# Kernel optimization log

Measured on AMD Instinct MI355X. Metric: run time of the kernel, lower is better.

Reference implementation:

```python
import jax, jax.numpy as jnp
import numpy as np

UNITS = 1024
D_Q = 1024
D_V = 1024


def setup_inputs() -> dict:
    key = jax.random.key(0)
    ks = jax.random.split(key, 8)
    B, S = 32, 2048
    query = jax.random.normal(ks[0], (B, D_Q), dtype=jnp.float32)
    values = jax.random.normal(ks[1], (B, S, D_V), dtype=jnp.float32)
    # Keras Dense params (glorot-ish scale for weights, zero bias init kept random-free)
    W1 = jax.random.normal(ks[2], (D_V, UNITS), dtype=jnp.float32) / np.sqrt(D_V)
    b1 = jnp.zeros((UNITS,), dtype=jnp.float32)
    W2 = jax.random.normal(ks[3], (D_Q, UNITS), dtype=jnp.float32) / np.sqrt(D_Q)
    b2 = jnp.zeros((UNITS,), dtype=jnp.float32)
    V = jax.random.normal(ks[4], (UNITS, 1), dtype=jnp.float32) / np.sqrt(UNITS)
    bV = jnp.zeros((1,), dtype=jnp.float32)
    return {"query": query, "values": values, "W1": W1, "b1": b1,
            "W2": W2, "b2": b2, "V": V, "bV": bV}


def reference(query, values, W1, b1, W2, b2, V, bV):
    # query: [B, d_q], values: [B, S, d_v]
    proj_v = jnp.einsum('bsd,du->bsu', values, W1) + b1        # [B, S, U]
    proj_q = (query @ W2 + b2)[:, None, :]                      # [B, 1, U]
    score = jnp.tanh(proj_v + proj_q) @ V + bV                  # [B, S, 1]
    attention_weights = jax.nn.softmax(score, axis=1)           # [B, S, 1]
    context_vector = jnp.sum(attention_weights * values, axis=1)  # [B, d_v]
    return (context_vector, attention_weights)
```

## Files before the change

### kernel.cpp

```cpp
#include <hip/hip_runtime.h>
#include <math.h>

#define B_  32
#define S_  2048
#define DV  1024
#define U_  1024

typedef __attribute__((ext_vector_type(8))) short bf16x8;
typedef __attribute__((ext_vector_type(4))) float f32x4;

__device__ inline unsigned short f2bf(float f) {
    unsigned int x = __float_as_uint(f);
    return (unsigned short)((x + 0x7fffu + ((x >> 16) & 1u)) >> 16);
}

__device__ inline float tanh_fast(float x) {
    float ax = fabsf(x);
    float e  = __expf(ax + ax);
    float t  = 1.0f - __fdividef(2.0f, e + 1.0f);
    return copysignf(t, x);
}

__device__ __forceinline__ void gload16(const void* g, void* l) {
    __builtin_amdgcn_global_load_lds(
        (const __attribute__((address_space(1))) void*)g,
        (__attribute__((address_space(3))) void*)l,
        16, 0, 0);
}

#define ASM_VMCNT(N) asm volatile("s_waitcnt vmcnt(" #N ")" ::: "memory")
#define ASM_LGKM0()  do { asm volatile("s_waitcnt lgkmcnt(0)" ::: "memory"); \
                          __builtin_amdgcn_sched_barrier(0); } while (0)

__global__ __launch_bounds__(256)
void fused_prep(const float* __restrict__ values, char* __restrict__ AbfT,
                const float* __restrict__ W1, unsigned short* __restrict__ W1T,
                const float* __restrict__ query, const float* __restrict__ W2,
                const float* __restrict__ b1, const float* __restrict__ b2,
                float* __restrict__ t, float* __restrict__ scores,
                float* __restrict__ ctx) {
    const int bid = blockIdx.x;
    const int tid = threadIdx.x;

    if (bid < 32768) {
        size_t i = ((size_t)bid * 256 + tid) * 8;
        int row = (int)(i >> 10);
        int k   = (int)(i & 1023);
        float4 f0 = *(const float4*)(values + i);
        float4 f1 = *(const float4*)(values + i + 4);
        union { unsigned short s[8]; uint4 u; } p;
        p.s[0] = f2bf(f0.x); p.s[1] = f2bf(f0.y); p.s[2] = f2bf(f0.z); p.s[3] = f2bf(f0.w);
        p.s[4] = f2bf(f1.x); p.s[5] = f2bf(f1.y); p.s[6] = f2bf(f1.z); p.s[7] = f2bf(f1.w);
        int stile = row >> 8, rt = row & 255, h = rt >> 7, r = rt & 127;
        int kt = k >> 6, kk = k & 63;
        int pchunk = (kk >> 3) ^ (r & 7);
        size_t dst = (size_t)stile * 524288 + (size_t)kt * 32768
                   + h * 16384 + r * 128 + pchunk * 16;
        *(uint4*)(AbfT + dst) = p.u;
    } else if (bid < 33024) {
        __shared__ float tile[64][65];
        int i = bid - 32768;
        int k0 = (i & 15) * 64, u0 = (i >> 4) * 64;
        int lr = tid >> 4, lc = (tid & 15) * 4;
#pragma unroll
        for (int j = 0; j < 4; ++j) {
            float4 f = *(const float4*)&W1[(size_t)(k0 + lr + j * 16) * U_ + u0 + lc];
            tile[lr + j * 16][lc + 0] = f.x; tile[lr + j * 16][lc + 1] = f.y;
            tile[lr + j * 16][lc + 2] = f.z; tile[lr + j * 16][lc + 3] = f.w;
        }
        __syncthreads();
        int ur = tid >> 2, kq = (tid & 3) * 16;
        union { unsigned short s[8]; uint4 u; } p0, p1;
#pragma unroll
        for (int e = 0; e < 8; ++e) p0.s[e] = f2bf(tile[kq + e][ur]);
#pragma unroll
        for (int e = 0; e < 8; ++e) p1.s[e] = f2bf(tile[kq + 8 + e][ur]);
        unsigned short* dst = W1T + (size_t)(u0 + ur) * 1024 + k0 + kq;
        *(uint4*)dst       = p0.u;
        *(uint4*)(dst + 8) = p1.u;
    } else if (bid < 33152) {
        __shared__ float qs2[1024];
        int i = bid - 33024;
        int b = i >> 2, uq = i & 3;
        for (int j = tid; j < 1024; j += 256) qs2[j] = query[b * DV + j];
        __syncthreads();
        int u = uq * 256 + tid;
        float a0 = 0.f, a1 = 0.f, a2 = 0.f, a3 = 0.f;
        float a4 = 0.f, a5 = 0.f, a6 = 0.f, a7 = 0.f;
        const float* w = W2 + u;
        for (int k = 0; k < 1024; k += 8) {
            a0 += qs2[k + 0] * w[(size_t)(k + 0) * U_];
            a1 += qs2[k + 1] * w[(size_t)(k + 1) * U_];
            a2 += qs2[k + 2] * w[(size_t)(k + 2) * U_];
            a3 += qs2[k + 3] * w[(size_t)(k + 3) * U_];
            a4 += qs2[k + 4] * w[(size_t)(k + 4) * U_];
            a5 += qs2[k + 5] * w[(size_t)(k + 5) * U_];
            a6 += qs2[k + 6] * w[(size_t)(k + 6) * U_];
            a7 += qs2[k + 7] * w[(size_t)(k + 7) * U_];
        }
        t[b * U_ + u] = b1[u] + b2[u]
                      + ((a0 + a1) + (a2 + a3)) + ((a4 + a5) + (a6 + a7));
    } else if (bid < 33408) {
        scores[(bid - 33152) * 256 + tid] = 0.f;
    } else {
        ctx[(bid - 33408) * 256 + tid] = 0.f;
    }
}

#define MFMA16(MB, NB)                                                          \
    _Pragma("unroll") for (int ks = 0; ks < 2; ++ks)                            \
    _Pragma("unroll") for (int n = 0; n < 2; ++n)                               \
    _Pragma("unroll") for (int m = 0; m < 4; ++m)                               \
        acc[(MB)+m][(NB)+n] = __builtin_amdgcn_mfma_f32_16x16x32_bf16(          \
            af[m][ks], bf[n][ks], acc[(MB)+m][(NB)+n], 0, 0, 0);

__launch_bounds__(512, 2)
__global__ void scores_mfma8(const char* __restrict__ AbfT,
                             const unsigned short* __restrict__ W1T,
                             const float* __restrict__ tvec,
                             const float* __restrict__ V,
                             float* __restrict__ scores) {
    __shared__ __align__(16) char lds[131072];

    const int tid  = threadIdx.x;
    const int lane = tid & 63;
    const int wave = tid >> 6;
    const int wm   = wave >> 2;
    const int wn   = wave & 3;
    const int l15  = lane & 15;
    const int lq   = lane >> 4;

    const int id    = blockIdx.x;
    const int wg    = (id & 7) * 128 + (id >> 3);
    const int utile = wg & 3;
    const int stile = wg >> 2;
    const size_t row0 = (size_t)stile * 256;
    const int b       = (int)(row0 >> 11);
    const int s_local = (int)(row0 & 2047);
    const int u0      = utile * 256;

    const char* aBase = AbfT + (size_t)stile * 524288 + wave * 1024 + lane * 16;
    const int rowst = wave * 8 + (lane >> 3);
    const int kch8  = ((lane & 7) ^ ((lane >> 3) & 7)) * 8;
    const unsigned short* bSrc = W1T + (size_t)(u0 + rowst) * 1024 + kch8;
    char* const dstW = lds + wave * 1024;

    const int ao0 = wm * 16384 + l15 * 128 + ((lq ^ (l15 & 7)) << 4);
    const int ao1 = ao0 ^ 64;
    const int bo0 = 32768 + (wn >> 1) * 16384 + (wn & 1) * 8192
                  + l15 * 128 + ((lq ^ (l15 & 7)) << 4);
    const int bo1 = bo0 ^ 64;

    f32x4 acc[8][4];
#pragma unroll
    for (int m = 0; m < 8; ++m)
#pragma unroll
        for (int n = 0; n < 4; ++n) acc[m][n] = (f32x4)0.f;

    bf16x8 af[4][2];
    bf16x8 bf[2][2];

    auto stageA = [&](size_t gOff, int dOff) {
        gload16(aBase + gOff,        dstW + dOff);
        gload16(aBase + gOff + 8192, dstW + dOff + 8192);
    };
    auto stageB = [&](const unsigned short* s, int dOff) {
        gload16(s,             dstW + dOff);
        gload16(s + 64 * 1024, dstW + dOff + 8192);
    };
    auto readA4 = [&](int base) {
#pragma unroll
        for (int m = 0; m < 4; ++m) {
            af[m][0] = *(const bf16x8*)(lds + base + m * 2048 + ao0);
            af[m][1] = *(const bf16x8*)(lds + base + m * 2048 + ao1);
        }
    };
    auto readB2 = [&](int base) {
#pragma unroll
        for (int n = 0; n < 2; ++n) {
            bf[n][0] = *(const bf16x8*)(lds + base + n * 2048 + bo0);
            bf[n][1] = *(const bf16x8*)(lds + base + n * 2048 + bo1);
        }
    };

    stageA(0,     0);
    stageA(16384, 16384);
    stageB(bSrc,          32768);
    stageB(bSrc + 131072, 49152);
    stageA(32768, 65536);
    __builtin_amdgcn_sched_barrier(0);
    ASM_VMCNT(2);
    __builtin_amdgcn_s_barrier();
    __builtin_amdgcn_sched_barrier(0);

    for (int it = 0; it < 8; ++it) {
        const bool pf = (it < 7);
        const size_t aIt = (size_t)it * 65536;
        readA4(0);
        readB2(0);
        stageA(aIt + 49152, 81920);
        __builtin_amdgcn_s_barrier();
        ASM_LGKM0();
        __builtin_amdgcn_s_setprio(1);
        MFMA16(0, 0);
        __builtin_amdgcn_s_setprio(0);
        __builtin_amdgcn_s_barrier();
        readB2(2 * 2048);
        stageB(bSrc + 64, 98304);
        __builtin_amdgcn_s_barrier();
        ASM_LGKM0();
        __builtin_amdgcn_s_setprio(1);
        MFMA16(0, 2);
        __builtin_amdgcn_s_setprio(0);
        __builtin_amdgcn_s_barrier();
        readA4(4 * 2048);
        stageB(bSrc + 64 + 131072, 114688);
        __builtin_amdgcn_s_barrier();
        ASM_LGKM0();
        __builtin_amdgcn_s_setprio(1);
        MFMA16(4, 2);
        __builtin_amdgcn_s_setprio(0);
        __builtin_amdgcn_s_barrier();
        readB2(0);
        if (pf) stageA(aIt + 65536, 0);
        __builtin_amdgcn_s_barrier();
        ASM_LGKM0();
        __builtin_amdgcn_s_setprio(1);
        MFMA16(4, 0);
        __builtin_amdgcn_s_setprio(0);
        __builtin_amdgcn_sched_barrier(0);
        if (pf) { ASM_VMCNT(2); } else { ASM_VMCNT(0); }
        __builtin_amdgcn_s_barrier();
        __builtin_amdgcn_sched_barrier(0);
        readA4(65536);
        readB2(65536);
        if (pf) stageA(aIt + 81920, 16384);
        __builtin_amdgcn_s_barrier();
        ASM_LGKM0();
        __builtin_amdgcn_s_setprio(1);
        MFMA16(0, 0);
        __builtin_amdgcn_s_setprio(0);
        __builtin_amdgcn_s_barrier();
        readB2(65536 + 2 * 2048);
        if (pf) stageB(bSrc + 128, 32768);
        __builtin_amdgcn_s_barrier();
        ASM_LGKM0();
        __builtin_amdgcn_s_setprio(1);
        MFMA16(0, 2);
        __builtin_amdgcn_s_setprio(0);
        __builtin_amdgcn_s_barrier();
        readA4(65536 + 4 * 2048);
        if (pf) stageB(bSrc + 128 + 131072, 49152);
        __builtin_amdgcn_s_barrier();
        ASM_LGKM0();
        __builtin_amdgcn_s_setprio(1);
        MFMA16(4, 2);
        __builtin_amdgcn_s_setprio(0);
        __builtin_amdgcn_s_barrier();
        readB2(65536);
        if (pf) stageA(aIt + 98304, 65536);
        __builtin_amdgcn_s_barrier();
        ASM_LGKM0();
        __builtin_amdgcn_s_setprio(1);
        MFMA16(4, 0);
        __builtin_amdgcn_s_setprio(0);
        __builtin_amdgcn_sched_barrier(0);
        if (pf) { ASM_VMCNT(2); }
        __builtin_amdgcn_s_barrier();
        __builtin_amdgcn_sched_barrier(0);

        bSrc += 128;
    }

    __syncthreads();
    float* fscore = (float*)lds;
    if (tid < 256) fscore[tid] = 0.f;
    __syncthreads();
    float tu[4], vu[4];
#pragma unroll
    for (int n = 0; n < 4; ++n) {
        int u = u0 + wn * 64 + n * 16 + l15;
        tu[n] = tvec[b * U_ + u];
        vu[n] = V[u];
    }
#pragma unroll
    for (int m = 0; m < 8; ++m) {
#pragma unroll
        for (int r = 0; r < 4; ++r) {
            float p = 0.f;
#pragma unroll
            for (int n = 0; n < 4; ++n) p += tanh_fast(acc[m][n][r] + tu[n]) * vu[n];
            p += __shfl_xor(p, 1);
            p += __shfl_xor(p, 2);
            p += __shfl_xor(p, 4);
            p += __shfl_xor(p, 8);
            if (l15 == 0) atomicAdd(&fscore[wm * 128 + m * 16 + lq * 4 + r], p);
        }
    }
    __syncthreads();
    if (tid < 256) atomicAdd(&scores[(size_t)b * S_ + s_local + tid], fscore[tid]);
}

__global__ __launch_bounds__(256)
void fused_sm_ctx(const float* __restrict__ scores, const float* __restrict__ values,
                  float* __restrict__ wout, float* __restrict__ ctx) {
    const int b   = blockIdx.x;
    const int sc  = blockIdx.y;
    const int tid = threadIdx.x;
    __shared__ float red[256];
    __shared__ float ws_[128];

    float v[8];
    float m = -1e30f;
#pragma unroll
    for (int i = 0; i < 8; ++i) {
        v[i] = scores[(size_t)b * S_ + tid + i * 256];
        m = fmaxf(m, v[i]);
    }
    red[tid] = m; __syncthreads();
    for (int off = 128; off > 0; off >>= 1) {
        if (tid < off) red[tid] = fmaxf(red[tid], red[tid + off]);
        __syncthreads();
    }
    m = red[0];
    __syncthreads();
    float s = 0.f;
#pragma unroll
    for (int i = 0; i < 8; ++i) s += __expf(v[i] - m);
    red[tid] = s; __syncthreads();
    for (int off = 128; off > 0; off >>= 1) {
        if (tid < off) red[tid] += red[tid + off];
        __syncthreads();
    }
    float inv = 1.f / red[0];
    __syncthreads();

    if (tid < 128) {
        float x = scores[(size_t)b * S_ + sc * 128 + tid];
        float w = __expf(x - m) * inv;
        ws_[tid] = w;
        wout[(size_t)b * S_ + sc * 128 + tid] = w;
    }
    __syncthreads();

    const float4* vp = (const float4*)(values + ((size_t)b * S_ + sc * 128) * DV) + tid;
    float ax = 0.f, ay = 0.f, az = 0.f, aw = 0.f;
#pragma unroll 4
    for (int s2 = 0; s2 < 128; ++s2) {
        float4 vv = vp[(size_t)s2 * 256];
        float wv = ws_[s2];
        ax += wv * vv.x; ay += wv * vv.y; az += wv * vv.z; aw += wv * vv.w;
    }
    float* c = ctx + b * DV + tid * 4;
    atomicAdd(c + 0, ax); atomicAdd(c + 1, ay);
    atomicAdd(c + 2, az); atomicAdd(c + 3, aw);
}

__global__ void init_kernel(const float* __restrict__ b1, const float* __restrict__ b2,
                            float* __restrict__ t, float* __restrict__ ctx,
                            float* __restrict__ scores) {
    int i = blockIdx.x * 256 + threadIdx.x;
    scores[i] = 0.f;
    if (i < B_ * U_) {
        int u = i & (U_ - 1);
        t[i]   = b1[u] + b2[u];
        ctx[i] = 0.f;
    }
}

__global__ void projq_kernel(const float* __restrict__ q, const float* __restrict__ W2,
                             float* __restrict__ t) {
    int b  = blockIdx.x;
    int ks = blockIdx.y;
    int tid = threadIdx.x;
    __shared__ float qs[64];
    if (tid < 64) qs[tid] = q[b * DV + ks * 64 + tid];
    __syncthreads();
    float a0 = 0.f, a1 = 0.f, a2 = 0.f, a3 = 0.f;
    const float* w = W2 + (size_t)(ks * 64) * U_;
    for (int d = 0; d < 64; ++d) {
        float qd = qs[d];
        const float* wr = w + (size_t)d * U_ + tid;
        a0 += qd * wr[0];
        a1 += qd * wr[256];
        a2 += qd * wr[512];
        a3 += qd * wr[768];
    }
    atomicAdd(&t[b * U_ + tid      ], a0);
    atomicAdd(&t[b * U_ + tid + 256], a1);
    atomicAdd(&t[b * U_ + tid + 512], a2);
    atomicAdd(&t[b * U_ + tid + 768], a3);
}

__global__ void prep_w1t(const float* __restrict__ W1, unsigned short* __restrict__ W1T) {
    __shared__ float tile[64][65];
    int k0 = blockIdx.x * 64, u0 = blockIdx.y * 64;
    int t = threadIdx.x;
    int lr = t >> 4, lc = (t & 15) * 4;
#pragma unroll
    for (int i = 0; i < 4; ++i) {
        float4 f = *(const float4*)&W1[(size_t)(k0 + lr + i * 16) * U_ + u0 + lc];
        tile[lr + i * 16][lc + 0] = f.x; tile[lr + i * 16][lc + 1] = f.y;
        tile[lr + i * 16][lc + 2] = f.z; tile[lr + i * 16][lc + 3] = f.w;
    }
    __syncthreads();
    int ur = t >> 2, kq = (t & 3) * 16;
    union { unsigned short s[8]; uint4 u; } p0, p1;
#pragma unroll
    for (int e = 0; e < 8; ++e) p0.s[e] = f2bf(tile[kq + e][ur]);
#pragma unroll
    for (int e = 0; e < 8; ++e) p1.s[e] = f2bf(tile[kq + 8 + e][ur]);
    unsigned short* dst = W1T + (size_t)(u0 + ur) * 1024 + k0 + kq;
    *(uint4*)dst       = p0.u;
    *(uint4*)(dst + 8) = p1.u;
}

template<bool ABF16>
__launch_bounds__(256, 2)
__global__ void scores_mfma(const void* __restrict__ aPtr,
                            const unsigned short* __restrict__ W1T,
                            const float* __restrict__ t,
                            const float* __restrict__ V,
                            float* __restrict__ scores) {
    __shared__ unsigned short sA[128 * 40];
    __shared__ unsigned short sB[256 * 40];
    __shared__ float fscore[128];

    const int tid  = threadIdx.x;
    const int lane = tid & 63;
    const int wave = tid >> 6;
    const int wm = wave & 1, wn = wave >> 1;
    const int l15 = lane & 15, lq = lane >> 4;

    const int id    = blockIdx.x;
    const int utile = (id >> 3) & 3;
    const int stile = (id & 7) | ((id >> 5) << 3);
    const size_t row0 = (size_t)stile * 128;
    const int b       = (int)(row0 >> 11);
    const int s_local = (int)(row0 & 2047);
    const int u0      = utile * 256;

    if (tid < 128) fscore[tid] = 0.f;

    const int ar = tid >> 1, ak = (tid & 1) << 4;
    const int br = tid >> 1, bk = (tid & 1) << 4;

    const float* Af = (const float*)aPtr + (row0 + ar) * 1024 + ak;
    const unsigned short* Ab = (const unsigned short*)aPtr + (row0 + ar) * 1024 + ak;
    const unsigned short* Bp0 = W1T + (size_t)(u0 + br) * 1024 + bk;
    const unsigned short* Bp1 = Bp0 + 128 * 1024;

    f32x4 acc[4][8];
#pragma unroll
    for (int i = 0; i < 4; ++i)
#pragma unroll
        for (int j = 0; j < 8; ++j) acc[i][j] = (f32x4)0.f;

    uint4 sa0, sa1, sb0, sb1, sb2, sb3;
    float4 fa0, fa1, fa2, fa3;

    if (ABF16) {
        sa0 = *(const uint4*)(Ab);
        sa1 = *(const uint4*)(Ab + 8);
    } else {
        fa0 = *(const float4*)(Af);
        fa1 = *(const float4*)(Af + 4);
        fa2 = *(const float4*)(Af + 8);
        fa3 = *(const float4*)(Af + 12);
    }
    sb0 = *(const uint4*)(Bp0);
    sb1 = *(const uint4*)(Bp0 + 8);
    sb2 = *(const uint4*)(Bp1);
    sb3 = *(const uint4*)(Bp1 + 8);

    for (int k0 = 0; k0 < 1024; k0 += 32) {
        __syncthreads();
        if (ABF16) {
            *(uint4*)&sA[ar * 40 + ak]     = sa0;
            *(uint4*)&sA[ar * 40 + ak + 8] = sa1;
        } else {
            union { unsigned short s[8]; uint4 u; } p0, p1;
            p0.s[0] = f2bf(fa0.x); p0.s[1] = f2bf(fa0.y); p0.s[2] = f2bf(fa0.z); p0.s[3] = f2bf(fa0.w);
            p0.s[4] = f2bf(fa1.x); p0.s[5] = f2bf(fa1.y); p0.s[6] = f2bf(fa1.z); p0.s[7] = f2bf(fa1.w);
            p1.s[0] = f2bf(fa2.x); p1.s[1] = f2bf(fa2.y); p1.s[2] = f2bf(fa2.z); p1.s[3] = f2bf(fa2.w);
            p1.s[4] = f2bf(fa3.x); p1.s[5] = f2bf(fa3.y); p1.s[6] = f2bf(fa3.z); p1.s[7] = f2bf(fa3.w);
            *(uint4*)&sA[ar * 40 + ak]     = p0.u;
            *(uint4*)&sA[ar * 40 + ak + 8] = p1.u;
        }
        *(uint4*)&sB[br * 40 + bk]           = sb0;
        *(uint4*)&sB[br * 40 + bk + 8]       = sb1;
        *(uint4*)&sB[(br + 128) * 40 + bk]     = sb2;
        *(uint4*)&sB[(br + 128) * 40 + bk + 8] = sb3;

        if (k0 + 32 < 1024) {
            int nk = k0 + 32;
            if (ABF16) {
                sa0 = *(const uint4*)(Ab + nk);
                sa1 = *(const uint4*)(Ab + nk + 8);
            } else {
                fa0 = *(const float4*)(Af + nk);
                fa1 = *(const float4*)(Af + nk + 4);
                fa2 = *(const float4*)(Af + nk + 8);
                fa3 = *(const float4*)(Af + nk + 12);
            }
            sb0 = *(const uint4*)(Bp0 + nk);
            sb1 = *(const uint4*)(Bp0 + nk + 8);
            sb2 = *(const uint4*)(Bp1 + nk);
            sb3 = *(const uint4*)(Bp1 + nk + 8);
        }
        __syncthreads();

        bf16x8 af[4];
#pragma unroll
        for (int i = 0; i < 4; ++i)
            af[i] = *(const bf16x8*)&sA[(64 * wm + 16 * i + l15) * 40 + lq * 8];
#pragma unroll
        for (int j = 0; j < 8; ++j) {
            bf16x8 bfj = *(const bf16x8*)&sB[(128 * wn + 16 * j + l15) * 40 + lq * 8];
#pragma unroll
            for (int i = 0; i < 4; ++i)
                acc[i][j] = __builtin_amdgcn_mfma_f32_16x16x32_bf16(af[i], bfj, acc[i][j], 0, 0, 0);
        }
    }

    float tu[8], vu[8];
#pragma unroll
    for (int j = 0; j < 8; ++j) {
        int u = u0 + 128 * wn + 16 * j + l15;
        tu[j] = t[b * U_ + u];
        vu[j] = V[u];
    }
#pragma unroll
    for (int i = 0; i < 4; ++i) {
#pragma unroll
        for (int r = 0; r < 4; ++r) {
            float p = 0.f;
#pragma unroll
            for (int j = 0; j < 8; ++j) p += tanh_fast(acc[i][j][r] + tu[j]) * vu[j];
            p += __shfl_xor(p, 1);
            p += __shfl_xor(p, 2);
            p += __shfl_xor(p, 4);
            p += __shfl_xor(p, 8);
            if (l15 == 0) atomicAdd(&fscore[64 * wm + 16 * i + lq * 4 + r], p);
        }
    }
    __syncthreads();
    if (tid < 128) atomicAdd(&scores[(size_t)b * S_ + s_local + tid], fscore[tid]);
}

__launch_bounds__(256, 2)
__global__ void scores_vec(const float* __restrict__ values, const float* __restrict__ W1,
                           const float* __restrict__ t, const float* __restrict__ V,
                           float* __restrict__ scores) {
    __shared__ float vA[16][132];
    __shared__ float vB[16][68];
    __shared__ float fscore[128];
    const int b   = blockIdx.y;
    const int s0  = blockIdx.x * 128;
    const int tid = threadIdx.x;
    const int tx  = tid & 15, ty = tid >> 4;
    if (tid < 128) fscore[tid] = 0.f;
    const float* vbase = values + ((size_t)b * S_ + s0) * (size_t)DV;
    const int lm = tid >> 2, lkq = (tid & 3) * 4;
    const int lbk = tid >> 4, lbj = (tid & 15) * 4;
    for (int nt = 0; nt < U_ / 64; ++nt) {
        const int u0 = nt * 64;
        float acc[8][4];
#pragma unroll
        for (int i = 0; i < 8; ++i)
#pragma unroll
            for (int j = 0; j < 4; ++j) acc[i][j] = 0.f;
        for (int k0 = 0; k0 < DV; k0 += 16) {
            __syncthreads();
            const float4 v0 = *(const float4*)(vbase + (size_t)lm * DV + k0 + lkq);
            const float4 v1 = *(const float4*)(vbase + (size_t)(lm + 64) * DV + k0 + lkq);
            vA[lkq + 0][lm] = v0.x; vA[lkq + 1][lm] = v0.y;
            vA[lkq + 2][lm] = v0.z; vA[lkq + 3][lm] = v0.w;
            vA[lkq + 0][lm + 64] = v1.x; vA[lkq + 1][lm + 64] = v1.y;
            vA[lkq + 2][lm + 64] = v1.z; vA[lkq + 3][lm + 64] = v1.w;
            *(float4*)&vB[lbk][lbj] = *(const float4*)(W1 + (size_t)(k0 + lbk) * U_ + u0 + lbj);
            __syncthreads();
#pragma unroll
            for (int k = 0; k < 16; ++k) {
                float4 va0 = *(const float4*)&vA[k][ty * 8];
                float4 va1 = *(const float4*)&vA[k][ty * 8 + 4];
                float4 vb  = *(const float4*)&vB[k][tx * 4];
                float a_[8] = {va0.x, va0.y, va0.z, va0.w, va1.x, va1.y, va1.z, va1.w};
                float b_[4] = {vb.x, vb.y, vb.z, vb.w};
#pragma unroll
                for (int i = 0; i < 8; ++i)
#pragma unroll
                    for (int j = 0; j < 4; ++j) acc[i][j] += a_[i] * b_[j];
            }
        }
        float tq[4], vv[4];
#pragma unroll
        for (int j = 0; j < 4; ++j) {
            int u = u0 + tx * 4 + j;
            tq[j] = t[b * U_ + u];
            vv[j] = V[u];
        }
#pragma unroll
        for (int i = 0; i < 8; ++i) {
            float p = 0.f;
#pragma unroll
            for (int j = 0; j < 4; ++j) p += tanhf(acc[i][j] + tq[j]) * vv[j];
            p += __shfl_down(p, 8, 16);
            p += __shfl_down(p, 4, 16);
            p += __shfl_down(p, 2, 16);
            p += __shfl_down(p, 1, 16);
            if (tx == 0) fscore[ty * 8 + i] += p;
        }
    }
    __syncthreads();
    if (tid < 128) scores[(size_t)b * S_ + s0 + tid] = fscore[tid];
}

__global__ void softmax_kernel(const float* __restrict__ scores, float* __restrict__ wout) {
    int b = blockIdx.x;
    int tid = threadIdx.x;
    __shared__ float red[256];
    float v[8];
    float m = -1e30f;
#pragma unroll
    for (int i = 0; i < 8; ++i) {
        v[i] = scores[(size_t)b * S_ + tid + i * 256];
        m = fmaxf(m, v[i]);
    }
    red[tid] = m; __syncthreads();
    for (int off = 128; off > 0; off >>= 1) {
        if (tid < off) red[tid] = fmaxf(red[tid], red[tid + off]);
        __syncthreads();
    }
    m = red[0];
    __syncthreads();
    float s = 0.f;
#pragma unroll
    for (int i = 0; i < 8; ++i) { v[i] = __expf(v[i] - m); s += v[i]; }
    red[tid] = s; __syncthreads();
    for (int off = 128; off > 0; off >>= 1) {
        if (tid < off) red[tid] += red[tid + off];
        __syncthreads();
    }
    float inv = 1.f / red[0];
#pragma unroll
    for (int i = 0; i < 8; ++i) wout[(size_t)b * S_ + tid + i * 256] = v[i] * inv;
}

__global__ void context_kernel(const float* __restrict__ values, const float* __restrict__ w,
                               float* __restrict__ ctx) {
    int b   = blockIdx.x;
    int sc  = blockIdx.y;
    int tid = threadIdx.x;
    __shared__ float ws_[128];
    if (tid < 128) ws_[tid] = w[(size_t)b * S_ + sc * 128 + tid];
    __syncthreads();
    const float4* vp = (const float4*)(values + ((size_t)b * S_ + sc * 128) * DV) + tid;
    float ax = 0.f, ay = 0.f, az = 0.f, aw = 0.f;
#pragma unroll 4
    for (int s = 0; s < 128; ++s) {
        float4 v = vp[(size_t)s * 256];
        float wv = ws_[s];
        ax += wv * v.x; ay += wv * v.y; az += wv * v.z; aw += wv * v.w;
    }
    float* c = ctx + b * DV + tid * 4;
    atomicAdd(c + 0, ax); atomicAdd(c + 1, ay);
    atomicAdd(c + 2, az); atomicAdd(c + 3, aw);
}

extern "C" void kernel_launch(void* const* d_in, const int* in_sizes, int n_in,
                              void* d_out, int out_size, void* d_ws, size_t ws_size,
                              hipStream_t stream) {
    const float* query  = (const float*)d_in[0];
    const float* values = (const float*)d_in[1];
    const float* W1     = (const float*)d_in[2];
    const float* b1     = (const float*)d_in[3];
    const float* W2     = (const float*)d_in[4];
    const float* b2     = (const float*)d_in[5];
    const float* V      = (const float*)d_in[6];

    float* out  = (float*)d_out;
    float* ctx  = out;
    float* wout = out + B_ * DV;

    char* ws = (char*)d_ws;
    const size_t W1T_BYTES = (size_t)U_ * DV * 2;
    const size_t T_BYTES   = (size_t)B_ * U_ * 4;
    const size_t SC_BYTES  = (size_t)B_ * S_ * 4;
    const size_t ABF_BYTES = (size_t)B_ * S_ * DV * 2;

    if (ws_size >= W1T_BYTES + T_BYTES + SC_BYTES + ABF_BYTES) {
        unsigned short* W1T = (unsigned short*)ws;
        float* t      = (float*)(ws + W1T_BYTES);
        float* scores = t + B_ * U_;
        char*  AbfT   = (char*)(scores + B_ * S_);

        fused_prep  <<<dim3(33536),   256, 0, stream>>>(values, AbfT, W1, W1T,
                                                        query, W2, b1, b2,
                                                        t, scores, ctx);
        scores_mfma8<<<dim3(1024),    512, 0, stream>>>(AbfT, W1T, t, V, scores);
        fused_sm_ctx<<<dim3(32, 16),  256, 0, stream>>>(scores, values, wout, ctx);
    } else if (ws_size >= W1T_BYTES + T_BYTES + SC_BYTES) {
        unsigned short* W1T = (unsigned short*)ws;
        float* t      = (float*)(ws + W1T_BYTES);
        float* scores = t + B_ * U_;

        init_kernel   <<<dim3(256),      256, 0, stream>>>(b1, b2, t, ctx, scores);
        projq_kernel  <<<dim3(32, 16),   256, 0, stream>>>(query, W2, t);
        prep_w1t      <<<dim3(16, 16),   256, 0, stream>>>(W1, W1T);
        scores_mfma<false><<<dim3(2048), 256, 0, stream>>>(values, W1T, t, V, scores);
        softmax_kernel<<<dim3(32),       256, 0, stream>>>(scores, wout);
        context_kernel<<<dim3(32, 16),   256, 0, stream>>>(values, wout, ctx);
    } else {
        float* t      = (float*)ws;
        float* scores = t + B_ * U_;

        init_kernel   <<<dim3(256),      256, 0, stream>>>(b1, b2, t, ctx, scores);
        projq_kernel  <<<dim3(32, 16),   256, 0, stream>>>(query, W2, t);
        scores_vec    <<<dim3(16, 32),   256, 0, stream>>>(values, W1, t, V, scores);
        softmax_kernel<<<dim3(32),       256, 0, stream>>>(scores, wout);
        context_kernel<<<dim3(32, 16),   256, 0, stream>>>(values, wout, ctx);
    }
}
```

Baseline: 616.1 us.

## Fuse fp32-to-bf16 conversion of values into the MFMA scores kernel

Removes the separate pre-pass that converted the full values tensor to a swizzled bf16 copy in workspace. The scores GEMM kernel now loads fp32 values into registers, packs them to bf16 and writes them into swizzled LDS itself, with the prefetch and wait schedule reworked around the register staging. This is meant to save the 256MB read plus 128MB write of the conversion pass. In exchange the GEMM reads twice the A bytes, uses more registers and does conversion ALU work in its main loop, and the old fallback path is removed.

```diff
diff --git a/kernel.cpp b/kernel.cpp
--- a/kernel.cpp
+++ b/kernel.cpp
@@ -12,6 +12,13 @@
 __device__ inline unsigned short f2bf(float f) {
     unsigned int x = __float_as_uint(f);
     return (unsigned short)((x + 0x7fffu + ((x >> 16) & 1u)) >> 16);
+}
+
+__device__ inline uint4 pack8(float4 a, float4 b) {
+    union { unsigned short s[8]; uint4 u; } p;
+    p.s[0] = f2bf(a.x); p.s[1] = f2bf(a.y); p.s[2] = f2bf(a.z); p.s[3] = f2bf(a.w);
+    p.s[4] = f2bf(b.x); p.s[5] = f2bf(b.y); p.s[6] = f2bf(b.z); p.s[7] = f2bf(b.w);
+    return p.u;
 }
 
 __device__ inline float tanh_fast(float x) {
@@ -33,8 +40,7 @@
                           __builtin_amdgcn_sched_barrier(0); } while (0)
 
 __global__ __launch_bounds__(256)
-void fused_prep(const float* __restrict__ values, char* __restrict__ AbfT,
-                const float* __restrict__ W1, unsigned short* __restrict__ W1T,
+void prep_small(const float* __restrict__ W1, unsigned short* __restrict__ W1T,
                 const float* __restrict__ query, const float* __restrict__ W2,
                 const float* __restrict__ b1, const float* __restrict__ b2,
                 float* __restrict__ t, float* __restrict__ scores,
@@ -42,25 +48,9 @@
     const int bid = blockIdx.x;
     const int tid = threadIdx.x;
 
-    if (bid < 32768) {
-        size_t i = ((size_t)bid * 256 + tid) * 8;
-        int row = (int)(i >> 10);
-        int k   = (int)(i & 1023);
-        float4 f0 = *(const float4*)(values + i);
-        float4 f1 = *(const float4*)(values + i + 4);
-        union { unsigned short s[8]; uint4 u; } p;
-        p.s[0] = f2bf(f0.x); p.s[1] = f2bf(f0.y); p.s[2] = f2bf(f0.z); p.s[3] = f2bf(f0.w);
-        p.s[4] = f2bf(f1.x); p.s[5] = f2bf(f1.y); p.s[6] = f2bf(f1.z); p.s[7] = f2bf(f1.w);
-        int stile = row >> 8, rt = row & 255, h = rt >> 7, r = rt & 127;
-        int kt = k >> 6, kk = k & 63;
-        int pchunk = (kk >> 3) ^ (r & 7);
-        size_t dst = (size_t)stile * 524288 + (size_t)kt * 32768
-                   + h * 16384 + r * 128 + pchunk * 16;
-        *(uint4*)(AbfT + dst) = p.u;
-    } else if (bid < 33024) {
+    if (bid < 256) {
         __shared__ float tile[64][65];
-        int i = bid - 32768;
-        int k0 = (i & 15) * 64, u0 = (i >> 4) * 64;
+        int k0 = (bid & 15) * 64, u0 = (bid >> 4) * 64;
         int lr = tid >> 4, lc = (tid & 15) * 4;
 #pragma unroll
         for (int j = 0; j < 4; ++j) {
@@ -78,9 +68,9 @@
         unsigned short* dst = W1T + (size_t)(u0 + ur) * 1024 + k0 + kq;
         *(uint4*)dst       = p0.u;
         *(uint4*)(dst + 8) = p1.u;
-    } else if (bid < 33152) {
+    } else if (bid < 384) {
         __shared__ float qs2[1024];
-        int i = bid - 33024;
+        int i = bid - 256;
         int b = i >> 2, uq = i & 3;
         for (int j = tid; j < 1024; j += 256) qs2[j] = query[b * DV + j];
         __syncthreads();
@@ -100,10 +90,10 @@
         }
         t[b * U_ + u] = b1[u] + b2[u]
                       + ((a0 + a1) + (a2 + a3)) + ((a4 + a5) + (a6 + a7));
-    } else if (bid < 33408) {
-        scores[(bid - 33152) * 256 + tid] = 0.f;
+    } else if (bid < 640) {
+        scores[(bid - 384) * 256 + tid] = 0.f;
     } else {
-        ctx[(bid - 33408) * 256 + tid] = 0.f;
+        ctx[(bid - 640) * 256 + tid] = 0.f;
     }
 }
 
@@ -114,12 +104,20 @@
         acc[(MB)+m][(NB)+n] = __builtin_amdgcn_mfma_f32_16x16x32_bf16(          \
             af[m][ks], bf[n][ks], acc[(MB)+m][(NB)+n], 0, 0, 0);
 
+#define ISSUEA(Sa, Sb, Sc, Sd, kt, h) do {                                      \
+    const float4* _s = (const float4*)(aRow + (size_t)(h) * 131072 + (kt) * 64);\
+    Sa = _s[0]; Sb = _s[1]; Sc = _s[2]; Sd = _s[3]; } while (0)
+
+#define WRITEA(Sa, Sb, Sc, Sd, dOff) do {                                       \
+    *(uint4*)(lds + (dOff) + wO0) = pack8(Sa, Sb);                              \
+    *(uint4*)(lds + (dOff) + wO1) = pack8(Sc, Sd); } while (0)
+
 __launch_bounds__(512, 2)
-__global__ void scores_mfma8(const char* __restrict__ AbfT,
-                             const unsigned short* __restrict__ W1T,
-                             const float* __restrict__ tvec,
-                             const float* __restrict__ V,
-                             float* __restrict__ scores) {
+__global__ void scores_mfma8f(const float* __restrict__ values,
+                              const unsigned short* __restrict__ W1T,
+                              const float* __restrict__ tvec,
+                              const float* __restrict__ V,
+                              float* __restrict__ scores) {
     __shared__ __align__(16) char lds[131072];
 
     const int tid  = threadIdx.x;
@@ -139,11 +137,17 @@
     const int s_local = (int)(row0 & 2047);
     const int u0      = utile * 256;
 
-    const char* aBase = AbfT + (size_t)stile * 524288 + wave * 1024 + lane * 16;
     const int rowst = wave * 8 + (lane >> 3);
     const int kch8  = ((lane & 7) ^ ((lane >> 3) & 7)) * 8;
     const unsigned short* bSrc = W1T + (size_t)(u0 + rowst) * 1024 + kch8;
     char* const dstW = lds + wave * 1024;
+
+    const int rA  = tid >> 2;
+    const int kcA = tid & 3;
+    const int c0  = (2 * kcA) ^ (rA & 7);
+    const int wO0 = rA * 128 + c0 * 16;
+    const int wO1 = rA * 128 + (c0 ^ 1) * 16;
+    const float* aRow = values + (row0 + rA) * 1024 + kcA * 16;
 
     const int ao0 = wm * 16384 + l15 * 128 + ((lq ^ (l15 & 7)) << 4);
     const int ao1 = ao0 ^ 64;
@@ -160,10 +164,6 @@
     bf16x8 af[4][2];
     bf16x8 bf[2][2];
 
-    auto stageA = [&](size_t gOff, int dOff) {
-        gload16(aBase + gOff,        dstW + dOff);
-        gload16(aBase + gOff + 8192, dstW + dOff + 8192);
-    };
     auto stageB = [&](const unsigned short* s, int dOff) {
         gload16(s,             dstW + dOff);
         gload16(s + 64 * 1024, dstW + dOff + 8192);
@@ -183,38 +183,48 @@
         }
     };
 
-    stageA(0,     0);
-    stageA(16384, 16384);
+    float4 s0a, s0b, s0c, s0d;
+    float4 s1a, s1b, s1c, s1d;
+    float4 s2a, s2b, s2c, s2d;
+
+    ISSUEA(s0a, s0b, s0c, s0d, 0, 0);
+    ISSUEA(s2a, s2b, s2c, s2d, 0, 1);
     stageB(bSrc,          32768);
     stageB(bSrc + 131072, 49152);
-    stageA(32768, 65536);
-    __builtin_amdgcn_sched_barrier(0);
-    ASM_VMCNT(2);
+    ISSUEA(s1a, s1b, s1c, s1d, 1, 0);
+    ASM_VMCNT(8);
+    WRITEA(s0a, s0b, s0c, s0d, 0);
+    WRITEA(s2a, s2b, s2c, s2d, 16384);
+    ASM_VMCNT(4);
+    ASM_LGKM0();
     __builtin_amdgcn_s_barrier();
     __builtin_amdgcn_sched_barrier(0);
 
     for (int it = 0; it < 8; ++it) {
         const bool pf = (it < 7);
-        const size_t aIt = (size_t)it * 65536;
+        ISSUEA(s0a, s0b, s0c, s0d, 2 * it + 1, 1);
+        ASM_VMCNT(4);
+        WRITEA(s1a, s1b, s1c, s1d, 65536);
         readA4(0);
         readB2(0);
-        stageA(aIt + 49152, 81920);
         __builtin_amdgcn_s_barrier();
         ASM_LGKM0();
         __builtin_amdgcn_s_setprio(1);
         MFMA16(0, 0);
         __builtin_amdgcn_s_setprio(0);
         __builtin_amdgcn_s_barrier();
+        stageB(bSrc + 64, 98304);
+        ASM_VMCNT(2);
+        WRITEA(s0a, s0b, s0c, s0d, 81920);
         readB2(2 * 2048);
-        stageB(bSrc + 64, 98304);
         __builtin_amdgcn_s_barrier();
         ASM_LGKM0();
         __builtin_amdgcn_s_setprio(1);
         MFMA16(0, 2);
         __builtin_amdgcn_s_setprio(0);
         __builtin_amdgcn_s_barrier();
+        stageB(bSrc + 64 + 131072, 114688);
         readA4(4 * 2048);
-        stageB(bSrc + 64 + 131072, 114688);
         __builtin_amdgcn_s_barrier();
         ASM_LGKM0();
         __builtin_amdgcn_s_setprio(1);
@@ -222,19 +232,23 @@
         __builtin_amdgcn_s_setprio(0);
         __builtin_amdgcn_s_barrier();
         readB2(0);
-        if (pf) stageA(aIt + 65536, 0);
+        if (pf) ISSUEA(s1a, s1b, s1c, s1d, 2 * it + 2, 0);
         __builtin_amdgcn_s_barrier();
         ASM_LGKM0();
         __builtin_amdgcn_s_setprio(1);
         MFMA16(4, 0);
         __builtin_amdgcn_s_setprio(0);
         __builtin_amdgcn_sched_barrier(0);
-        if (pf) { ASM_VMCNT(2); } else { ASM_VMCNT(0); }
+        if (pf) { ASM_VMCNT(4); } else { ASM_VMCNT(0); }
         __builtin_amdgcn_s_barrier();
         __builtin_amdgcn_sched_barrier(0);
+        if (pf) {
+            ISSUEA(s0a, s0b, s0c, s0d, 2 * it + 2, 1);
+            ASM_VMCNT(4);
+            WRITEA(s1a, s1b, s1c, s1d, 0);
+        }
         readA4(65536);
         readB2(65536);
-        if (pf) stageA(aIt + 81920, 16384);
         __builtin_amdgcn_s_barrier();
         ASM_LGKM0();
         __builtin_amdgcn_s_setprio(1);
@@ -242,15 +256,19 @@
         __builtin_amdgcn_s_setprio(0);
         __builtin_amdgcn_s_barrier();
         readB2(65536 + 2 * 2048);
-        if (pf) stageB(bSrc + 128, 32768);
+        if (pf) {
+            stageB(bSrc + 128, 32768);
+            ASM_VMCNT(2);
+            WRITEA(s0a, s0b, s0c, s0d, 16384);
+        }
         __builtin_amdgcn_s_barrier();
         ASM_LGKM0();
         __builtin_amdgcn_s_setprio(1);
         MFMA16(0, 2);
         __builtin_amdgcn_s_setprio(0);
         __builtin_amdgcn_s_barrier();
+        if (pf) stageB(bSrc + 128 + 131072, 49152);
         readA4(65536 + 4 * 2048);
-        if (pf) stageB(bSrc + 128 + 131072, 49152);
         __builtin_amdgcn_s_barrier();
         ASM_LGKM0();
         __builtin_amdgcn_s_setprio(1);
@@ -258,14 +276,14 @@
         __builtin_amdgcn_s_setprio(0);
         __builtin_amdgcn_s_barrier();
         readB2(65536);
-        if (pf) stageA(aIt + 98304, 65536);
+        if (pf) ISSUEA(s1a, s1b, s1c, s1d, 2 * it + 3, 0);
         __builtin_amdgcn_s_barrier();
         ASM_LGKM0();
         __builtin_amdgcn_s_setprio(1);
         MFMA16(4, 0);
         __builtin_amdgcn_s_setprio(0);
         __builtin_amdgcn_sched_barrier(0);
-        if (pf) { ASM_VMCNT(2); }
+        if (pf) { ASM_VMCNT(4); }
         __builtin_amdgcn_s_barrier();
         __builtin_amdgcn_sched_barrier(0);
 
@@ -390,162 +408,6 @@
     atomicAdd(&t[b * U_ + tid + 256], a1);
     atomicAdd(&t[b * U_ + tid + 512], a2);
     atomicAdd(&t[b * U_ + tid + 768], a3);
-}
-
-__global__ void prep_w1t(const float* __restrict__ W1, unsigned short* __restrict__ W1T) {
-    __shared__ float tile[64][65];
-    int k0 = blockIdx.x * 64, u0 = blockIdx.y * 64;
-    int t = threadIdx.x;
-    int lr = t >> 4, lc = (t & 15) * 4;
-#pragma unroll
-    for (int i = 0; i < 4; ++i) {
-        float4 f = *(const float4*)&W1[(size_t)(k0 + lr + i * 16) * U_ + u0 + lc];
-        tile[lr + i * 16][lc + 0] = f.x; tile[lr + i * 16][lc + 1] = f.y;
-        tile[lr + i * 16][lc + 2] = f.z; tile[lr + i * 16][lc + 3] = f.w;
-    }
-    __syncthreads();
-    int ur = t >> 2, kq = (t & 3) * 16;
-    union { unsigned short s[8]; uint4 u; } p0, p1;
-#pragma unroll
-    for (int e = 0; e < 8; ++e) p0.s[e] = f2bf(tile[kq + e][ur]);
-#pragma unroll
-    for (int e = 0; e < 8; ++e) p1.s[e] = f2bf(tile[kq + 8 + e][ur]);
-    unsigned short* dst = W1T + (size_t)(u0 + ur) * 1024 + k0 + kq;
-    *(uint4*)dst       = p0.u;
-    *(uint4*)(dst + 8) = p1.u;
-}
-
-template<bool ABF16>
-__launch_bounds__(256, 2)
-__global__ void scores_mfma(const void* __restrict__ aPtr,
-                            const unsigned short* __restrict__ W1T,
-                            const float* __restrict__ t,
-                            const float* __restrict__ V,
-                            float* __restrict__ scores) {
-    __shared__ unsigned short sA[128 * 40];
-    __shared__ unsigned short sB[256 * 40];
-    __shared__ float fscore[128];
-
-    const int tid  = threadIdx.x;
-    const int lane = tid & 63;
-    const int wave = tid >> 6;
-    const int wm = wave & 1, wn = wave >> 1;
-    const int l15 = lane & 15, lq = lane >> 4;
-
-    const int id    = blockIdx.x;
-    const int utile = (id >> 3) & 3;
-    const int stile = (id & 7) | ((id >> 5) << 3);
-    const size_t row0 = (size_t)stile * 128;
-    const int b       = (int)(row0 >> 11);
-    const int s_local = (int)(row0 & 2047);
-    const int u0      = utile * 256;
-
-    if (tid < 128) fscore[tid] = 0.f;
-
-    const int ar = tid >> 1, ak = (tid & 1) << 4;
-    const int br = tid >> 1, bk = (tid & 1) << 4;
-
-    const float* Af = (const float*)aPtr + (row0 + ar) * 1024 + ak;
-    const unsigned short* Ab = (const unsigned short*)aPtr + (row0 + ar) * 1024 + ak;
-    const unsigned short* Bp0 = W1T + (size_t)(u0 + br) * 1024 + bk;
-    const unsigned short* Bp1 = Bp0 + 128 * 1024;
-
-    f32x4 acc[4][8];
-#pragma unroll
-    for (int i = 0; i < 4; ++i)
-#pragma unroll
-        for (int j = 0; j < 8; ++j) acc[i][j] = (f32x4)0.f;
-
-    uint4 sa0, sa1, sb0, sb1, sb2, sb3;
-    float4 fa0, fa1, fa2, fa3;
-
-    if (ABF16) {
-        sa0 = *(const uint4*)(Ab);
-        sa1 = *(const uint4*)(Ab + 8);
-    } else {
-        fa0 = *(const float4*)(Af);
-        fa1 = *(const float4*)(Af + 4);
-        fa2 = *(const float4*)(Af + 8);
-        fa3 = *(const float4*)(Af + 12);
-    }
-    sb0 = *(const uint4*)(Bp0);
-    sb1 = *(const uint4*)(Bp0 + 8);
-    sb2 = *(const uint4*)(Bp1);
-    sb3 = *(const uint4*)(Bp1 + 8);
-
-    for (int k0 = 0; k0 < 1024; k0 += 32) {
-        __syncthreads();
-        if (ABF16) {
-            *(uint4*)&sA[ar * 40 + ak]     = sa0;
-            *(uint4*)&sA[ar * 40 + ak + 8] = sa1;
-        } else {
-            union { unsigned short s[8]; uint4 u; } p0, p1;
-            p0.s[0] = f2bf(fa0.x); p0.s[1] = f2bf(fa0.y); p0.s[2] = f2bf(fa0.z); p0.s[3] = f2bf(fa0.w);
-            p0.s[4] = f2bf(fa1.x); p0.s[5] = f2bf(fa1.y); p0.s[6] = f2bf(fa1.z); p0.s[7] = f2bf(fa1.w);
-            p1.s[0] = f2bf(fa2.x); p1.s[1] = f2bf(fa2.y); p1.s[2] = f2bf(fa2.z); p1.s[3] = f2bf(fa2.w);
-            p1.s[4] = f2bf(fa3.x); p1.s[5] = f2bf(fa3.y); p1.s[6] = f2bf(fa3.z); p1.s[7] = f2bf(fa3.w);
-            *(uint4*)&sA[ar * 40 + ak]     = p0.u;
-            *(uint4*)&sA[ar * 40 + ak + 8] = p1.u;
-        }
-        *(uint4*)&sB[br * 40 + bk]           = sb0;
-        *(uint4*)&sB[br * 40 + bk + 8]       = sb1;
-        *(uint4*)&sB[(br + 128) * 40 + bk]     = sb2;
-        *(uint4*)&sB[(br + 128) * 40 + bk + 8] = sb3;
-
-        if (k0 + 32 < 1024) {
-            int nk = k0 + 32;
-            if (ABF16) {
-                sa0 = *(const uint4*)(Ab + nk);
-                sa1 = *(const uint4*)(Ab + nk + 8);
-            } else {
-                fa0 = *(const float4*)(Af + nk);
-                fa1 = *(const float4*)(Af + nk + 4);
-                fa2 = *(const float4*)(Af + nk + 8);
-                fa3 = *(const float4*)(Af + nk + 12);
-            }
-            sb0 = *(const uint4*)(Bp0 + nk);
-            sb1 = *(const uint4*)(Bp0 + nk + 8);
-            sb2 = *(const uint4*)(Bp1 + nk);
-            sb3 = *(const uint4*)(Bp1 + nk + 8);
-        }
-        __syncthreads();
-
-        bf16x8 af[4];
-#pragma unroll
-        for (int i = 0; i < 4; ++i)
-            af[i] = *(const bf16x8*)&sA[(64 * wm + 16 * i + l15) * 40 + lq * 8];
-#pragma unroll
-        for (int j = 0; j < 8; ++j) {
-            bf16x8 bfj = *(const bf16x8*)&sB[(128 * wn + 16 * j + l15) * 40 + lq * 8];
-#pragma unroll
-            for (int i = 0; i < 4; ++i)
-                acc[i][j] = __builtin_amdgcn_mfma_f32_16x16x32_bf16(af[i], bfj, acc[i][j], 0, 0, 0);
-        }
-    }
-
-    float tu[8], vu[8];
-#pragma unroll
-    for (int j = 0; j < 8; ++j) {
-        int u = u0 + 128 * wn + 16 * j + l15;
-        tu[j] = t[b * U_ + u];
-        vu[j] = V[u];
-    }
-#pragma unroll
-    for (int i = 0; i < 4; ++i) {
-#pragma unroll
-        for (int r = 0; r < 4; ++r) {
-            float p = 0.f;
-#pragma unroll
-            for (int j = 0; j < 8; ++j) p += tanh_fast(acc[i][j][r] + tu[j]) * vu[j];
-            p += __shfl_xor(p, 1);
-            p += __shfl_xor(p, 2);
-            p += __shfl_xor(p, 4);
-            p += __shfl_xor(p, 8);
-            if (l15 == 0) atomicAdd(&fscore[64 * wm + 16 * i + lq * 4 + r], p);
-        }
-    }
-    __syncthreads();
-    if (tid < 128) atomicAdd(&scores[(size_t)b * S_ + s_local + tid], fscore[tid]);
 }
 
 __launch_bounds__(256, 2)
@@ -687,30 +549,16 @@
     const size_t W1T_BYTES = (size_t)U_ * DV * 2;
     const size_t T_BYTES   = (size_t)B_ * U_ * 4;
     const size_t SC_BYTES  = (size_t)B_ * S_ * 4;
-    const size_t ABF_BYTES = (size_t)B_ * S_ * DV * 2;
-
-    if (ws_size >= W1T_BYTES + T_BYTES + SC_BYTES + ABF_BYTES) {
+
+    if (ws_size >= W1T_BYTES + T_BYTES + SC_BYTES) {
         unsigned short* W1T = (unsigned short*)ws;
         float* t      = (float*)(ws + W1T_BYTES);
         float* scores = t + B_ * U_;
-        char*  AbfT   = (char*)(scores + B_ * S_);
-
-        fused_prep  <<<dim3(33536),   256, 0, stream>>>(values, AbfT, W1, W1T,
-                                                        query, W2, b1, b2,
-                                                        t, scores, ctx);
-        scores_mfma8<<<dim3(1024),    512, 0, stream>>>(AbfT, W1T, t, V, scores);
-        fused_sm_ctx<<<dim3(32, 16),  256, 0, stream>>>(scores, values, wout, ctx);
-    } else if (ws_size >= W1T_BYTES + T_BYTES + SC_BYTES) {
-        unsigned short* W1T = (unsigned short*)ws;
-        float* t      = (float*)(ws + W1T_BYTES);
-        float* scores = t + B_ * U_;
-
-        init_kernel   <<<dim3(256),      256, 0, stream>>>(b1, b2, t, ctx, scores);
-        projq_kernel  <<<dim3(32, 16),   256, 0, stream>>>(query, W2, t);
-        prep_w1t      <<<dim3(16, 16),   256, 0, stream>>>(W1, W1T);
-        scores_mfma<false><<<dim3(2048), 256, 0, stream>>>(values, W1T, t, V, scores);
-        softmax_kernel<<<dim3(32),       256, 0, stream>>>(scores, wout);
-        context_kernel<<<dim3(32, 16),   256, 0, stream>>>(values, wout, ctx);
+
+        prep_small   <<<dim3(768),    256, 0, stream>>>(W1, W1T, query, W2,
+                                                        b1, b2, t, scores, ctx);
+        scores_mfma8f<<<dim3(1024),   512, 0, stream>>>(values, W1T, t, V, scores);
+        fused_sm_ctx <<<dim3(32, 16), 256, 0, stream>>>(scores, values, wout, ctx);
     } else {
         float* t      = (float*)ws;
         float* scores = t + B_ * U_;
```

Measured after the change: 660.9 us. 7.3% more time.
